# Kernel optimization log

Measured on AMD Instinct MI355X. Metric: run time of the kernel, lower is better.

Reference implementation:

```python
import jax, jax.numpy as jnp
import numpy as np

N, B, H, D = 8, 4, 16, 64   # batch, beam, heads, head_dim
T, S, L = 16, 1024, 1024    # new tokens, prefix len, past len
E = H * D
SCALE = 1.0 / np.sqrt(D).astype(np.float32)


def setup_inputs() -> dict:
    key = jax.random.key(0)
    ks = jax.random.split(key, 10)
    wscale = 1.0 / np.sqrt(E).astype(np.float32)
    return {
        "hidden_states": jax.random.normal(ks[0], (N * B, T, E), jnp.float32),
        "attention_mask": jnp.zeros((N * B, 1, 1, S + L + T), jnp.float32),
        "rel_pos": jax.random.normal(ks[1], (N * B, H, T, S + L + T), jnp.float32) * 0.1,
        "past_prefix_key": jax.random.normal(ks[2], (N, H, S, D), jnp.float32),
        "past_prefix_value": jax.random.normal(ks[3], (N, H, S, D), jnp.float32),
        "past_key": jax.random.normal(ks[4], (N * B, H, L, D), jnp.float32),
        "past_value": jax.random.normal(ks[5], (N * B, H, L, D), jnp.float32),
        "Wq": jax.random.normal(ks[6], (E, E), jnp.float32) * wscale,
        "bq": jnp.zeros((E,), jnp.float32),
        "Wk": jax.random.normal(ks[7], (E, E), jnp.float32) * wscale,
        "bk": jnp.zeros((E,), jnp.float32),
        "Wv": jax.random.normal(ks[8], (E, E), jnp.float32) * wscale,
        "bv": jnp.zeros((E,), jnp.float32),
    }


def _heads(x):
    # (NB, T, E) -> (NB, H, T, D)
    nb, t, _ = x.shape
    return x.reshape(nb, t, H, D).transpose(0, 2, 1, 3)


def reference(hidden_states, attention_mask, rel_pos, past_prefix_key,
              past_prefix_value, past_key, past_value, Wq, bq, Wk, bk, Wv, bv):
    q = _heads(hidden_states @ Wq.T + bq)   # (NB,H,T,D)
    k = _heads(hidden_states @ Wk.T + bk)
    v = _heads(hidden_states @ Wv.T + bv)

    # prefix scores: batch-shared prefix KV, per-beam queries
    q5 = q.reshape(N, B, H, T, D)
    prefix_scores = jnp.einsum('bxhtd,bhsd->bxhts', q5, past_prefix_key)
    prefix_scores = prefix_scores.reshape(N * B, H, T, S) * SCALE

    key_layer = jnp.concatenate([past_key, k], axis=2)      # (NB,H,L+T,D)
    value_layer = jnp.concatenate([past_value, v], axis=2)
    scores = jnp.einsum('bhtd,bhsd->bhts', q, key_layer) * SCALE

    scores = jnp.concatenate([prefix_scores, scores], axis=-1)  # (NB,H,T,S+L+T)
    scores = scores + rel_pos + attention_mask
    probs = jax.nn.softmax(scores, axis=-1)

    prefix_probs = probs[..., :S]
    rest_probs = probs[..., S:]

    prefix_ctx = jnp.einsum('bxhts,bhsd->bxhtd',
                            prefix_probs.reshape(N, B, H, T, S),
                            past_prefix_value).reshape(N * B, H, T, D)
    ctx = prefix_ctx + jnp.einsum('bhts,bhsd->bhtd', rest_probs, value_layer)

    # (NB,H,T,D) -> (NB,T,E)
    return ctx.transpose(0, 2, 1, 3).reshape(N * B, T, E)
```

## Files before the change

kernel.cpp:

```cpp
#include <hip/hip_runtime.h>

#define NH 16
#define NT 16
#define DD 64
#define SS 1024
#define LL 1024
#define TOTK 2064
#define EE 1024
#define NWAVE 8

typedef __attribute__((ext_vector_type(8))) short bf16x8;
typedef __attribute__((ext_vector_type(4))) float f32x4;

__device__ __forceinline__ unsigned short f2bf(float x) {
  union { float f; unsigned u; } v; v.f = x;
  unsigned r = v.u + 0x7fffu + ((v.u >> 16) & 1u);
  return (unsigned short)(r >> 16);
}
__device__ __forceinline__ unsigned pkbf(float a, float b) {
  unsigned r;
  asm("v_cvt_pk_bf16_f32 %0, %1, %2" : "=v"(r) : "v"(a), "v"(b));
  return r;
}
union BF8 { unsigned u[4]; bf16x8 v; };

__device__ __forceinline__ void dma16(const void* g, void* l) {
  __builtin_amdgcn_global_load_lds(
      (const __attribute__((address_space(1))) unsigned int*)g,
      (__attribute__((address_space(3))) unsigned int*)l, 16, 0, 0);
}

__global__ __launch_bounds__(256)
void proj_kernel(const float* __restrict__ hidden,
                 const float* __restrict__ Wq, const float* __restrict__ bq,
                 const float* __restrict__ Wk, const float* __restrict__ bk,
                 const float* __restrict__ Wv, const float* __restrict__ bv,
                 unsigned short* __restrict__ qws,
                 float* __restrict__ kws, float* __restrict__ vws)
{
  __shared__ alignas(16) unsigned short As[64][72];
  __shared__ alignas(16) unsigned short Bs[64][72];
  const int mtile = blockIdx.x;
  const int ntile = blockIdx.y;
  const int mat = ntile >> 4;
  const int h = ntile & 15;
  const float* Wm = (mat == 0) ? Wq : (mat == 1 ? Wk : Wv);
  const float* bm = (mat == 0) ? bq : (mat == 1 ? bk : bv);
  const int tid = threadIdx.x;
  const int lane = tid & 63, w = tid >> 6;
  const int lr = lane & 15, lg = lane >> 4;
  const int m0 = mtile * 64;

  const f32x4 fz = {0.f, 0.f, 0.f, 0.f};
  f32x4 acc[4];
  #pragma unroll
  for (int j = 0; j < 4; ++j) acc[j] = fz;

  const int srow = tid >> 4, sc4 = tid & 15;
  float4 Ar[4], Br[4];
  #pragma unroll
  for (int it = 0; it < 4; ++it) {
    Ar[it] = *(const float4*)(hidden + (m0 + srow + it * 16) * EE + sc4 * 4);
    Br[it] = *(const float4*)(Wm + (h * 64 + srow + it * 16) * EE + sc4 * 4);
  }

  for (int k0 = 0; k0 < EE; k0 += 64) {
    __syncthreads();
    #pragma unroll
    for (int it = 0; it < 4; ++it) {
      int row = srow + it * 16;
      float4 a = Ar[it], b = Br[it];
      *(uint2*)(&As[row][sc4 * 4]) = make_uint2(pkbf(a.x, a.y), pkbf(a.z, a.w));
      *(uint2*)(&Bs[row][sc4 * 4]) = make_uint2(pkbf(b.x, b.y), pkbf(b.z, b.w));
    }
    __syncthreads();
    int kn = k0 + 64;
    if (kn < EE) {
      #pragma unroll
      for (int it = 0; it < 4; ++it) {
        Ar[it] = *(const float4*)(hidden + (m0 + srow + it * 16) * EE + kn + sc4 * 4);
        Br[it] = *(const float4*)(Wm + (h * 64 + srow + it * 16) * EE + kn + sc4 * 4);
      }
    }
    #pragma unroll
    for (int hh = 0; hh < 2; ++hh) {
      bf16x8 a = *(const bf16x8*)(&As[w * 16 + lr][hh * 32 + lg * 8]);
      #pragma unroll
      for (int dt = 0; dt < 4; ++dt) {
        bf16x8 b = *(const bf16x8*)(&Bs[dt * 16 + lr][hh * 32 + lg * 8]);
        acc[dt] = __builtin_amdgcn_mfma_f32_16x16x32_bf16(a, b, acc[dt], 0, 0, 0);
      }
    }
  }

  #pragma unroll
  for (int dt = 0; dt < 4; ++dt)
    #pragma unroll
    for (int r = 0; r < 4; ++r) {
      int Mrow = m0 + w * 16 + lg * 4 + r;
      int nb = Mrow >> 4, t = Mrow & 15;
      int d = dt * 16 + lr;
      float val = acc[dt][r] + bm[h * 64 + d];
      int oi = ((nb * NH + h) * NT + t) * DD + d;
      if (mat == 0) qws[oi] = f2bf(val);
      else if (mat == 1) kws[oi] = val;
      else vws[oi] = val;
    }
}

__global__ __launch_bounds__(512, 2)
void prefix_attn_kernel(const float* __restrict__ mask, const float* __restrict__ rel,
                        const float* __restrict__ ppk, const float* __restrict__ ppv,
                        const unsigned short* __restrict__ qws,
                        float* __restrict__ pfn, float* __restrict__ pfd)
{
  __shared__ __align__(16) float SB[2 * 128 * 64];
  __shared__ __align__(16) unsigned short Pb[NWAVE][16][40];

  const int bidx = blockIdx.x;
  const int h = bidx & 15;
  const int sn = bidx >> 4;
  const int nn = sn & 7;
  const int s = sn >> 3;
  const int tid = threadIdx.x;
  const int lane = tid & 63, w = tid >> 6;
  const int lr = lane & 15, lg = lane >> 4;
  const int key0 = s * 512;

  bf16x8 aq[4][2];
  #pragma unroll
  for (int b = 0; b < 4; ++b) {
    const unsigned short* qb = qws + (((nn * 4 + b) * NH + h) * NT) * DD;
    aq[b][0] = *(const bf16x8*)(qb + lr * DD + lg * 8);
    aq[b][1] = *(const bf16x8*)(qb + lr * DD + lg * 8 + 32);
  }

  const f32x4 fz = {0.f, 0.f, 0.f, 0.f};
  f32x4 ctx[4][4];
  float ls[4][4];
  #pragma unroll
  for (int b = 0; b < 4; ++b)
    #pragma unroll
    for (int j = 0; j < 4; ++j) { ctx[b][j] = fz; ls[b][j] = 0.f; }

  auto kstage = [&](int c, int buf) {
    const float* ks = ppk + ((nn * NH + h) * SS + key0 + c * 128) * DD;
    float* Kb = SB + buf * 128 * 64;
    #pragma unroll
    for (int q = 0; q < 4; ++q) {
      int Lrow = w * 16 + q * 4 + (lane >> 4);
      int colb = (lane & 15) * 16;
      int scolb = colb ^ ((Lrow & 7) << 4);
      dma16((const char*)ks + Lrow * 256 + scolb, Kb + (w * 16 + q * 4) * 64);
    }
  };

  kstage(0, 0);
  kstage(1, 1);

  #pragma unroll
  for (int p = 0; p < 2; ++p) {
    const int cA = 2 * p;
    const int kbA = key0 + cA * 128 + w * 16;

    const float* vs = ppv + ((nn * NH + h) * SS + key0 + cA * 128) * DD;
    float vraw[32];
    #pragma unroll
    for (int dt = 0; dt < 4; ++dt)
      #pragma unroll
      for (int e = 0; e < 8; ++e) {
        int kslot = lg * 8 + e;
        int j = (kslot >> 4) * 128 + w * 16 + (kslot & 15);
        vraw[dt * 8 + e] = vs[j * DD + dt * 16 + lr];
      }

    __builtin_amdgcn_sched_barrier(0);
    asm volatile("s_waitcnt vmcnt(32)" ::: "memory");
    __builtin_amdgcn_sched_barrier(0);

    float rr[4][2][4]; float mk[4][2];
    #pragma unroll
    for (int b = 0; b < 4; ++b) {
      const float* relb = rel + (((nn * 4 + b) * NH + h) * NT) * TOTK;
      const float* mb = mask + (nn * 4 + b) * TOTK;
      #pragma unroll
      for (int r = 0; r < 4; ++r) {
        rr[b][0][r] = relb[(lg * 4 + r) * TOTK + kbA + lr];
        rr[b][1][r] = relb[(lg * 4 + r) * TOTK + kbA + 128 + lr];
      }
      mk[b][0] = mb[kbA + lr];
      mk[b][1] = mb[kbA + 128 + lr];
    }

    bf16x8 kbf[2][2];
    #pragma unroll
    for (int sub = 0; sub < 2; ++sub) {
      const char* Kb = (const char*)(SB + sub * 128 * 64);
      #pragma unroll
      for (int hh = 0; hh < 2; ++hh) {
        int c0 = (hh * 128 + lg * 32) ^ ((lr & 7) << 4);
        int c1 = (hh * 128 + lg * 32 + 16) ^ ((lr & 7) << 4);
        float4 v0 = *(const float4*)(Kb + (w * 16 + lr) * 256 + c0);
        float4 v1 = *(const float4*)(Kb + (w * 16 + lr) * 256 + c1);
        BF8 o;
        o.u[0] = pkbf(v0.x, v0.y); o.u[1] = pkbf(v0.z, v0.w);
        o.u[2] = pkbf(v1.x, v1.y); o.u[3] = pkbf(v1.z, v1.w);
        kbf[sub][hh] = o.v;
      }
    }

    __builtin_amdgcn_sched_barrier(0);
    if (p == 0) { kstage(2, 0); kstage(3, 1); }
    __builtin_amdgcn_sched_barrier(0);

    bf16x8 vb[4];
    #pragma unroll
    for (int dt = 0; dt < 4; ++dt) {
      BF8 o;
      #pragma unroll
      for (int q = 0; q < 4; ++q)
        o.u[q] = pkbf(vraw[dt * 8 + q * 2], vraw[dt * 8 + q * 2 + 1]);
      vb[dt] = o.v;
    }

    #pragma unroll
    for (int b = 0; b < 4; ++b) {
      f32x4 sA = fz, sB = fz;
      sA = __builtin_amdgcn_mfma_f32_16x16x32_bf16(aq[b][0], kbf[0][0], sA, 0, 0, 0);
      sA = __builtin_amdgcn_mfma_f32_16x16x32_bf16(aq[b][1], kbf[0][1], sA, 0, 0, 0);
      sB = __builtin_amdgcn_mfma_f32_16x16x32_bf16(aq[b][0], kbf[1][0], sB, 0, 0, 0);
      sB = __builtin_amdgcn_mfma_f32_16x16x32_bf16(aq[b][1], kbf[1][1], sB, 0, 0, 0);
      #pragma unroll
      for (int r = 0; r < 4; ++r) {
        float pA = __expf(sA[r] * 0.125f + rr[b][0][r] + mk[b][0]);
        float pB = __expf(sB[r] * 0.125f + rr[b][1][r] + mk[b][1]);
        ls[b][r] += pA + pB;
        Pb[w][lg * 4 + r][lr] = f2bf(pA);
        Pb[w][lg * 4 + r][16 + lr] = f2bf(pB);
      }
      bf16x8 pa = *(const bf16x8*)(&Pb[w][lr][lg * 8]);
      #pragma unroll
      for (int dt = 0; dt < 4; ++dt)
        ctx[b][dt] = __builtin_amdgcn_mfma_f32_16x16x32_bf16(pa, vb[dt], ctx[b][dt], 0, 0, 0);
    }
  }

  #pragma unroll
  for (int b = 0; b < 4; ++b)
    #pragma unroll
    for (int r = 0; r < 4; ++r) {
      #pragma unroll
      for (int o = 8; o >= 1; o >>= 1) ls[b][r] += __shfl_xor(ls[b][r], o, 16);
    }

  float* mgc = SB;
  float* mgl = SB + NWAVE * 16 * 64;
  for (int b = 0; b < 4; ++b) {
    __syncthreads();
    #pragma unroll
    for (int dt = 0; dt < 4; ++dt)
      #pragma unroll
      for (int r = 0; r < 4; ++r)
        mgc[(w * 16 + lg * 4 + r) * 64 + dt * 16 + lr] = ctx[b][dt][r];
    if (lr == 0) {
      #pragma unroll
      for (int r = 0; r < 4; ++r) mgl[w * 16 + lg * 4 + r] = ls[b][r];
    }
    __syncthreads();
    #pragma unroll
    for (int i = 0; i < 2; ++i) {
      int idx = i * 512 + tid;
      int t = idx >> 6, d = idx & 63;
      float num = 0.f, den = 0.f;
      #pragma unroll
      for (int ww = 0; ww < NWAVE; ++ww) {
        den += mgl[ww * 16 + t];
        num += mgc[(ww * 16 + t) * 64 + d];
      }
      pfn[((sn * 16 + h) * 4 + b) * 1024 + t * 64 + d] = num;
      if (d == 0) pfd[((sn * 16 + h) * 4 + b) * 16 + t] = den;
    }
  }
}

__global__ __launch_bounds__(512, 2)
void past_attn_kernel(const float* __restrict__ mask, const float* __restrict__ rel,
                      const float* __restrict__ pk, const float* __restrict__ pv,
                      const unsigned short* __restrict__ qws,
                      const float* __restrict__ kws, const float* __restrict__ vws,
                      const float* __restrict__ pfn, const float* __restrict__ pfd,
                      float* __restrict__ out)
{
  __shared__ __align__(16) float SB[2 * 128 * 64];
  __shared__ __align__(16) unsigned short Pb[NWAVE][16][40];

  const int wg = blockIdx.x;
  const int nb = wg >> 4, h = wg & 15;
  const int tid = threadIdx.x;
  const int lane = tid & 63, w = tid >> 6;
  const int lr = lane & 15, lg = lane >> 4;

  const unsigned short* qbase = qws + ((nb * NH + h) * NT) * DD;
  bf16x8 aq0 = *(const bf16x8*)(qbase + lr * DD + lg * 8);
  bf16x8 aq1 = *(const bf16x8*)(qbase + lr * DD + lg * 8 + 32);

  const float* relbase = rel + ((nb * NH + h) * NT) * TOTK;
  const float* mbase = mask + nb * TOTK;

  const f32x4 fz = {0.f, 0.f, 0.f, 0.f};
  f32x4 ctx[4];
  float ls[4];
  #pragma unroll
  for (int dt = 0; dt < 4; ++dt) ctx[dt] = fz;
  #pragma unroll
  for (int r = 0; r < 4; ++r) ls[r] = 0.f;

  auto kstage = [&](int c, int buf) {
    const float* ks = (c < 8) ? pk + ((nb * NH + h) * LL + c * 128) * DD
                              : kws + ((nb * NH + h) * NT) * DD;
    float* Kb = SB + buf * 128 * 64;
    #pragma unroll
    for (int q = 0; q < 4; ++q) {
      int Lrow = w * 16 + q * 4 + (lane >> 4);
      int colb = (lane & 15) * 16;
      int scolb = colb ^ ((Lrow & 7) << 4);
      int srow = (c == 8) ? (Lrow & 15) : Lrow;
      dma16((const char*)ks + srow * 256 + scolb, Kb + (w * 16 + q * 4) * 64);
    }
  };

  auto qk_sub = [&](const float* Kb, const float rr[4], float mv, int sub) {
    bf16x8 kbf[2];
    #pragma unroll
    for (int hh = 0; hh < 2; ++hh) {
      int c0 = (hh * 128 + lg * 32) ^ ((lr & 7) << 4);
      int c1 = (hh * 128 + lg * 32 + 16) ^ ((lr & 7) << 4);
      float4 v0 = *(const float4*)((const char*)Kb + (w * 16 + lr) * 256 + c0);
      float4 v1 = *(const float4*)((const char*)Kb + (w * 16 + lr) * 256 + c1);
      BF8 o;
      o.u[0] = pkbf(v0.x, v0.y); o.u[1] = pkbf(v0.z, v0.w);
      o.u[2] = pkbf(v1.x, v1.y); o.u[3] = pkbf(v1.z, v1.w);
      kbf[hh] = o.v;
    }
    f32x4 s = fz;
    s = __builtin_amdgcn_mfma_f32_16x16x32_bf16(aq0, kbf[0], s, 0, 0, 0);
    s = __builtin_amdgcn_mfma_f32_16x16x32_bf16(aq1, kbf[1], s, 0, 0, 0);
    #pragma unroll
    for (int r = 0; r < 4; ++r) {
      float p = __expf(s[r] * 0.125f + rr[r] + mv);
      ls[r] += p;
      Pb[w][lg * 4 + r][sub * 16 + lr] = f2bf(p);
    }
  };

  auto rel_load = [&](int cA, float (&rA)[4], float (&rB)[4], float& mA, float& mB) {
    int kbA = SS + cA * 128 + w * 16, kbB = kbA + 128;
    #pragma unroll
    for (int r = 0; r < 4; ++r) {
      rA[r] = relbase[(lg * 4 + r) * TOTK + kbA + lr];
      rB[r] = relbase[(lg * 4 + r) * TOTK + kbB + lr];
    }
    mA = mbase[kbA + lr];
    mB = mbase[kbB + lr];
  };

  auto pair_iter = [&](int p, float (&rA)[4], float (&rB)[4], float& mA, float& mB,
                       float (&rAn)[4], float (&rBn)[4], float& mAn, float& mBn) {
    const int cA = 2 * p;

    __builtin_amdgcn_sched_barrier(0);
    asm volatile("s_waitcnt vmcnt(10)" ::: "memory");
    __builtin_amdgcn_sched_barrier(0);

    const float* vs = pv + ((nb * NH + h) * LL + cA * 128) * DD;
    float vraw[32];
    #pragma unroll
    for (int dt = 0; dt < 4; ++dt)
      #pragma unroll
      for (int e = 0; e < 8; ++e) {
        int kslot = lg * 8 + e;
        int j = (kslot >> 4) * 128 + w * 16 + (kslot & 15);
        vraw[dt * 8 + e] = vs[j * DD + dt * 16 + lr];
      }
    __builtin_amdgcn_sched_barrier(0);

    qk_sub(SB, rA, mA, 0);
    qk_sub(SB + 128 * 64, rB, mB, 1);

    __builtin_amdgcn_sched_barrier(0);
    if (p < 3) {
      kstage(cA + 2, 0);
      kstage(cA + 3, 1);
      rel_load(cA + 2, rAn, rBn, mAn, mBn);
    } else {
      kstage(8, 0);
    }
    __builtin_amdgcn_sched_barrier(0);

    bf16x8 pa = *(const bf16x8*)(&Pb[w][lr][lg * 8]);
    #pragma unroll
    for (int dt = 0; dt < 4; ++dt) {
      BF8 o;
      #pragma unroll
      for (int q = 0; q < 4; ++q)
        o.u[q] = pkbf(vraw[dt * 8 + q * 2], vraw[dt * 8 + q * 2 + 1]);
      ctx[dt] = __builtin_amdgcn_mfma_f32_16x16x32_bf16(pa, o.v, ctx[dt], 0, 0, 0);
    }
  };

  kstage(0, 0);
  kstage(1, 1);
  float ra0[4], rb0[4], ma0, mb0, ra1[4], rb1[4], ma1, mb1;
  rel_load(0, ra0, rb0, ma0, mb0);
  ma1 = mb1 = 0.f; ra1[0]=ra1[1]=ra1[2]=ra1[3]=0.f; rb1[0]=rb1[1]=rb1[2]=rb1[3]=0.f;

  for (int p = 0; p < 4; p += 2) {
    pair_iter(p,     ra0, rb0, ma0, mb0, ra1, rb1, ma1, mb1);
    pair_iter(p + 1, ra1, rb1, ma1, mb1, ra0, rb0, ma0, mb0);
  }

  if (w == 0) {
    #pragma unroll
    for (int r = 0; r < 4; ++r) Pb[0][lg * 4 + r][16 + lr] = 0;
    const float* vs = vws + ((nb * NH + h) * NT) * DD;
    float vraw[32];
    #pragma unroll
    for (int dt = 0; dt < 4; ++dt)
      #pragma unroll
      for (int e = 0; e < 8; ++e) {
        int kslot = lg * 8 + e;
        vraw[dt * 8 + e] = (kslot < 16) ? vs[kslot * DD + dt * 16 + lr] : 0.f;
      }
    float rrT[4];
    #pragma unroll
    for (int r = 0; r < 4; ++r)
      rrT[r] = relbase[(lg * 4 + r) * TOTK + 2048 + lr];
    float mvT = mbase[2048 + lr];

    __builtin_amdgcn_sched_barrier(0);
    asm volatile("s_waitcnt vmcnt(0)" ::: "memory");
    __builtin_amdgcn_sched_barrier(0);

    qk_sub(SB, rrT, mvT, 0);

    bf16x8 pa = *(const bf16x8*)(&Pb[0][lr][lg * 8]);
    #pragma unroll
    for (int dt = 0; dt < 4; ++dt) {
      BF8 o;
      #pragma unroll
      for (int q = 0; q < 4; ++q)
        o.u[q] = pkbf(vraw[dt * 8 + q * 2], vraw[dt * 8 + q * 2 + 1]);
      ctx[dt] = __builtin_amdgcn_mfma_f32_16x16x32_bf16(pa, o.v, ctx[dt], 0, 0, 0);
    }
  }

  #pragma unroll
  for (int r = 0; r < 4; ++r) {
    #pragma unroll
    for (int o = 8; o >= 1; o >>= 1) ls[r] += __shfl_xor(ls[r], o, 16);
  }

  __syncthreads();
  float* mgc = SB;
  float* mgl = SB + NWAVE * 16 * 64;
  #pragma unroll
  for (int dt = 0; dt < 4; ++dt)
    #pragma unroll
    for (int r = 0; r < 4; ++r)
      mgc[(w * 16 + lg * 4 + r) * 64 + dt * 16 + lr] = ctx[dt][r];
  if (lr == 0) {
    #pragma unroll
    for (int r = 0; r < 4; ++r) mgl[w * 16 + lg * 4 + r] = ls[r];
  }
  __syncthreads();
  const int n = nb >> 2, b = nb & 3;
  #pragma unroll
  for (int i = 0; i < 2; ++i) {
    int idx = i * 512 + tid;
    int t = idx >> 6, d = idx & 63;
    float num = 0.f, den = 0.f;
    #pragma unroll
    for (int ww = 0; ww < NWAVE; ++ww) {
      den += mgl[ww * 16 + t];
      num += mgc[(ww * 16 + t) * 64 + d];
    }
    #pragma unroll
    for (int sp = 0; sp < 2; ++sp) {
      int pbase = (((sp * 8 + n) * 16 + h) * 4 + b);
      num += pfn[pbase * 1024 + t * 64 + d];
      den += pfd[pbase * 16 + t];
    }
    out[((nb * NT + t) * NH + h) * DD + d] = num / den;
  }
}

extern "C" void kernel_launch(void* const* d_in, const int* in_sizes, int n_in,
                              void* d_out, int out_size, void* d_ws, size_t ws_size,
                              hipStream_t stream) {
  const float* hidden = (const float*)d_in[0];
  const float* mask   = (const float*)d_in[1];
  const float* rel    = (const float*)d_in[2];
  const float* ppk    = (const float*)d_in[3];
  const float* ppv    = (const float*)d_in[4];
  const float* pk     = (const float*)d_in[5];
  const float* pv     = (const float*)d_in[6];
  const float* Wq     = (const float*)d_in[7];
  const float* bq     = (const float*)d_in[8];
  const float* Wk     = (const float*)d_in[9];
  const float* bk     = (const float*)d_in[10];
  const float* Wv     = (const float*)d_in[11];
  const float* bv     = (const float*)d_in[12];
  float* out = (float*)d_out;

  unsigned short* qws = (unsigned short*)d_ws;
  float* kws = (float*)((char*)d_ws + (1u << 20));
  float* vws = (float*)((char*)d_ws + 3u * (1u << 20));
  float* pfn = (float*)((char*)d_ws + 5u * (1u << 20));
  float* pfd = (float*)((char*)d_ws + 9u * (1u << 20));

  proj_kernel<<<dim3(8, 48), 256, 0, stream>>>(hidden, Wq, bq, Wk, bk, Wv, bv,
                                               qws, kws, vws);
  prefix_attn_kernel<<<dim3(256), 512, 0, stream>>>(mask, rel, ppk, ppv,
                                                    qws, pfn, pfd);
  past_attn_kernel<<<dim3(512), 512, 0, stream>>>(mask, rel, pk, pv,
                                                  qws, kws, vws, pfn, pfd, out);
}
```

Measured before the change: 110.0 us.

## Deepen past-attention K staging to four LDS buffers and prefetch V ahead

The past-attention kernel now keeps four K chunks in LDS and issues the K DMA for two chunks ahead. It also prefetches the next pair's V values and rel/mask into registers while the current pair is processed, aiming to hide global-load latency behind the MFMA work. This doubles LDS use to 128KB and lowers the launch bound to one block per CU, which cuts occupancy. The prefix kernel also loses its unroll and manual waitcnt scheduling in favour of a full drain per iteration, which could expose more load latency.

Result: slower. 122.6 us (+11.5%).

```diff
diff --git a/kernel.cpp b/kernel.cpp
--- a/kernel.cpp
+++ b/kernel.cpp
@@ -8,6 +8,7 @@
 #define TOTK 2064
 #define EE 1024
 #define NWAVE 8
+#define CH (128 * 64)
 
 typedef __attribute__((ext_vector_type(8))) short bf16x8;
 typedef __attribute__((ext_vector_type(4))) float f32x4;
@@ -29,6 +30,11 @@
       (const __attribute__((address_space(1))) unsigned int*)g,
       (__attribute__((address_space(3))) unsigned int*)l, 16, 0, 0);
 }
+#define SBAR() __builtin_amdgcn_sched_barrier(0)
+#define DRAIN() do { \
+    asm volatile("s_waitcnt vmcnt(0)" ::: "memory"); \
+    __builtin_amdgcn_sched_barrier(0); \
+  } while (0)
 
 __global__ __launch_bounds__(256)
 void proj_kernel(const float* __restrict__ hidden,
@@ -108,13 +114,13 @@
     }
 }
 
-__global__ __launch_bounds__(512, 2)
+__global__ __launch_bounds__(512, 1)
 void prefix_attn_kernel(const float* __restrict__ mask, const float* __restrict__ rel,
                         const float* __restrict__ ppk, const float* __restrict__ ppv,
                         const unsigned short* __restrict__ qws,
                         float* __restrict__ pfn, float* __restrict__ pfd)
 {
-  __shared__ __align__(16) float SB[2 * 128 * 64];
+  __shared__ __align__(16) float SB[2 * CH];
   __shared__ __align__(16) unsigned short Pb[NWAVE][16][40];
 
   const int bidx = blockIdx.x;
@@ -126,6 +132,7 @@
   const int lane = tid & 63, w = tid >> 6;
   const int lr = lane & 15, lg = lane >> 4;
   const int key0 = s * 512;
+  const f32x4 fz = {0.f, 0.f, 0.f, 0.f};
 
   bf16x8 aq[4][2];
   #pragma unroll
@@ -135,7 +142,6 @@
     aq[b][1] = *(const bf16x8*)(qb + lr * DD + lg * 8 + 32);
   }
 
-  const f32x4 fz = {0.f, 0.f, 0.f, 0.f};
   f32x4 ctx[4][4];
   float ls[4][4];
   #pragma unroll
@@ -145,7 +151,7 @@
 
   auto kstage = [&](int c, int buf) {
     const float* ks = ppk + ((nn * NH + h) * SS + key0 + c * 128) * DD;
-    float* Kb = SB + buf * 128 * 64;
+    float* Kb = SB + buf * CH;
     #pragma unroll
     for (int q = 0; q < 4; ++q) {
       int Lrow = w * 16 + q * 4 + (lane >> 4);
@@ -158,10 +164,11 @@
   kstage(0, 0);
   kstage(1, 1);
 
-  #pragma unroll
   for (int p = 0; p < 2; ++p) {
     const int cA = 2 * p;
     const int kbA = key0 + cA * 128 + w * 16;
+
+    DRAIN();
 
     const float* vs = ppv + ((nn * NH + h) * SS + key0 + cA * 128) * DD;
     float vraw[32];
@@ -173,11 +180,6 @@
         int j = (kslot >> 4) * 128 + w * 16 + (kslot & 15);
         vraw[dt * 8 + e] = vs[j * DD + dt * 16 + lr];
       }
-
-    __builtin_amdgcn_sched_barrier(0);
-    asm volatile("s_waitcnt vmcnt(32)" ::: "memory");
-    __builtin_amdgcn_sched_barrier(0);
-
     float rr[4][2][4]; float mk[4][2];
     #pragma unroll
     for (int b = 0; b < 4; ++b) {
@@ -195,7 +197,7 @@
     bf16x8 kbf[2][2];
     #pragma unroll
     for (int sub = 0; sub < 2; ++sub) {
-      const char* Kb = (const char*)(SB + sub * 128 * 64);
+      const char* Kb = (const char*)(SB + sub * CH);
       #pragma unroll
       for (int hh = 0; hh < 2; ++hh) {
         int c0 = (hh * 128 + lg * 32) ^ ((lr & 7) << 4);
@@ -209,9 +211,7 @@
       }
     }
 
-    __builtin_amdgcn_sched_barrier(0);
     if (p == 0) { kstage(2, 0); kstage(3, 1); }
-    __builtin_amdgcn_sched_barrier(0);
 
     bf16x8 vb[4];
     #pragma unroll
@@ -283,7 +283,7 @@
   }
 }
 
-__global__ __launch_bounds__(512, 2)
+__global__ __launch_bounds__(512, 1)
 void past_attn_kernel(const float* __restrict__ mask, const float* __restrict__ rel,
                       const float* __restrict__ pk, const float* __restrict__ pv,
                       const unsigned short* __restrict__ qws,
@@ -291,7 +291,7 @@
                       const float* __restrict__ pfn, const float* __restrict__ pfd,
                       float* __restrict__ out)
 {
-  __shared__ __align__(16) float SB[2 * 128 * 64];
+  __shared__ __align__(16) float SB[4 * CH];
   __shared__ __align__(16) unsigned short Pb[NWAVE][16][40];
 
   const int wg = blockIdx.x;
@@ -299,6 +299,7 @@
   const int tid = threadIdx.x;
   const int lane = tid & 63, w = tid >> 6;
   const int lr = lane & 15, lg = lane >> 4;
+  const f32x4 fz = {0.f, 0.f, 0.f, 0.f};
 
   const unsigned short* qbase = qws + ((nb * NH + h) * NT) * DD;
   bf16x8 aq0 = *(const bf16x8*)(qbase + lr * DD + lg * 8);
@@ -307,7 +308,6 @@
   const float* relbase = rel + ((nb * NH + h) * NT) * TOTK;
   const float* mbase = mask + nb * TOTK;
 
-  const f32x4 fz = {0.f, 0.f, 0.f, 0.f};
   f32x4 ctx[4];
   float ls[4];
   #pragma unroll
@@ -315,10 +315,10 @@
   #pragma unroll
   for (int r = 0; r < 4; ++r) ls[r] = 0.f;
 
-  auto kstage = [&](int c, int buf) {
+  auto kstage = [&](int c) {
     const float* ks = (c < 8) ? pk + ((nb * NH + h) * LL + c * 128) * DD
                               : kws + ((nb * NH + h) * NT) * DD;
-    float* Kb = SB + buf * 128 * 64;
+    float* Kb = SB + (c & 3) * CH;
     #pragma unroll
     for (int q = 0; q < 4; ++q) {
       int Lrow = w * 16 + q * 4 + (lane >> 4);
@@ -327,6 +327,18 @@
       int srow = (c == 8) ? (Lrow & 15) : Lrow;
       dma16((const char*)ks + srow * 256 + scolb, Kb + (w * 16 + q * 4) * 64);
     }
+  };
+
+  auto vload = [&](int p, float (&vraw)[32]) {
+    const float* vs = pv + ((nb * NH + h) * LL + 2 * p * 128) * DD;
+    #pragma unroll
+    for (int dt = 0; dt < 4; ++dt)
+      #pragma unroll
+      for (int e = 0; e < 8; ++e) {
+        int kslot = lg * 8 + e;
+        int j = (kslot >> 4) * 128 + w * 16 + (kslot & 15);
+        vraw[dt * 8 + e] = vs[j * DD + dt * 16 + lr];
+      }
   };
 
   auto qk_sub = [&](const float* Kb, const float rr[4], float mv, int sub) {
@@ -364,72 +376,64 @@
     mB = mbase[kbB + lr];
   };
 
-  auto pair_iter = [&](int p, float (&rA)[4], float (&rB)[4], float& mA, float& mB,
-                       float (&rAn)[4], float (&rBn)[4], float& mAn, float& mBn) {
+  auto pair_iter = [&](int p, float (&vrawC)[32], float (&rA)[4], float (&rB)[4],
+                       float& mA, float& mB,
+                       float (&vrawN)[32], float (&rAn)[4], float (&rBn)[4],
+                       float& mAn, float& mBn) {
     const int cA = 2 * p;
 
-    __builtin_amdgcn_sched_barrier(0);
-    asm volatile("s_waitcnt vmcnt(10)" ::: "memory");
-    __builtin_amdgcn_sched_barrier(0);
-
-    const float* vs = pv + ((nb * NH + h) * LL + cA * 128) * DD;
-    float vraw[32];
+    qk_sub(SB + (cA & 3) * CH, rA, mA, 0);
+    qk_sub(SB + ((cA + 1) & 3) * CH, rB, mB, 1);
+    SBAR();
+
+    if (p < 2)      { kstage(cA + 4); kstage(cA + 5); }
+    else if (p == 2){ kstage(8); }
+    SBAR();
+    if (p < 3) {
+      rel_load(cA + 2, rAn, rBn, mAn, mBn);
+      vload(p + 1, vrawN);
+    }
+    SBAR();
+
+    bf16x8 pa = *(const bf16x8*)(&Pb[w][lr][lg * 8]);
+    #pragma unroll
+    for (int dt = 0; dt < 4; ++dt) {
+      BF8 o;
+      #pragma unroll
+      for (int q = 0; q < 4; ++q)
+        o.u[q] = pkbf(vrawC[dt * 8 + q * 2], vrawC[dt * 8 + q * 2 + 1]);
+      ctx[dt] = __builtin_amdgcn_mfma_f32_16x16x32_bf16(pa, o.v, ctx[dt], 0, 0, 0);
+    }
+  };
+
+  kstage(0); kstage(1); kstage(2); kstage(3);
+  SBAR();
+  float ra0[4], rb0[4], ma0, mb0, ra1[4], rb1[4], ma1, mb1;
+  float vraw0[32], vraw1[32];
+  rel_load(0, ra0, rb0, ma0, mb0);
+  vload(0, vraw0);
+  ma1 = mb1 = 0.f; ra1[0]=ra1[1]=ra1[2]=ra1[3]=0.f; rb1[0]=rb1[1]=rb1[2]=rb1[3]=0.f;
+  #pragma unroll
+  for (int i = 0; i < 32; ++i) vraw1[i] = 0.f;
+  DRAIN();
+
+  for (int p = 0; p < 4; p += 2) {
+    pair_iter(p,     vraw0, ra0, rb0, ma0, mb0, vraw1, ra1, rb1, ma1, mb1);
+    pair_iter(p + 1, vraw1, ra1, rb1, ma1, mb1, vraw0, ra0, rb0, ma0, mb0);
+  }
+
+  if (w == 0) {
+    DRAIN();
+    #pragma unroll
+    for (int r = 0; r < 4; ++r) Pb[0][lg * 4 + r][16 + lr] = 0;
+    const float* vs = vws + ((nb * NH + h) * NT) * DD;
+    float vrawT[32];
     #pragma unroll
     for (int dt = 0; dt < 4; ++dt)
       #pragma unroll
       for (int e = 0; e < 8; ++e) {
         int kslot = lg * 8 + e;
-        int j = (kslot >> 4) * 128 + w * 16 + (kslot & 15);
-        vraw[dt * 8 + e] = vs[j * DD + dt * 16 + lr];
-      }
-    __builtin_amdgcn_sched_barrier(0);
-
-    qk_sub(SB, rA, mA, 0);
-    qk_sub(SB + 128 * 64, rB, mB, 1);
-
-    __builtin_amdgcn_sched_barrier(0);
-    if (p < 3) {
-      kstage(cA + 2, 0);
-      kstage(cA + 3, 1);
-      rel_load(cA + 2, rAn, rBn, mAn, mBn);
-    } else {
-      kstage(8, 0);
-    }
-    __builtin_amdgcn_sched_barrier(0);
-
-    bf16x8 pa = *(const bf16x8*)(&Pb[w][lr][lg * 8]);
-    #pragma unroll
-    for (int dt = 0; dt < 4; ++dt) {
-      BF8 o;
-      #pragma unroll
-      for (int q = 0; q < 4; ++q)
-        o.u[q] = pkbf(vraw[dt * 8 + q * 2], vraw[dt * 8 + q * 2 + 1]);
-      ctx[dt] = __builtin_amdgcn_mfma_f32_16x16x32_bf16(pa, o.v, ctx[dt], 0, 0, 0);
-    }
-  };
-
-  kstage(0, 0);
-  kstage(1, 1);
-  float ra0[4], rb0[4], ma0, mb0, ra1[4], rb1[4], ma1, mb1;
-  rel_load(0, ra0, rb0, ma0, mb0);
-  ma1 = mb1 = 0.f; ra1[0]=ra1[1]=ra1[2]=ra1[3]=0.f; rb1[0]=rb1[1]=rb1[2]=rb1[3]=0.f;
-
-  for (int p = 0; p < 4; p += 2) {
-    pair_iter(p,     ra0, rb0, ma0, mb0, ra1, rb1, ma1, mb1);
-    pair_iter(p + 1, ra1, rb1, ma1, mb1, ra0, rb0, ma0, mb0);
-  }
-
-  if (w == 0) {
-    #pragma unroll
-    for (int r = 0; r < 4; ++r) Pb[0][lg * 4 + r][16 + lr] = 0;
-    const float* vs = vws + ((nb * NH + h) * NT) * DD;
-    float vraw[32];
-    #pragma unroll
-    for (int dt = 0; dt < 4; ++dt)
-      #pragma unroll
-      for (int e = 0; e < 8; ++e) {
-        int kslot = lg * 8 + e;
-        vraw[dt * 8 + e] = (kslot < 16) ? vs[kslot * DD + dt * 16 + lr] : 0.f;
+        vrawT[dt * 8 + e] = (kslot < 16) ? vs[kslot * DD + dt * 16 + lr] : 0.f;
       }
     float rrT[4];
     #pragma unroll
@@ -437,10 +441,6 @@
       rrT[r] = relbase[(lg * 4 + r) * TOTK + 2048 + lr];
     float mvT = mbase[2048 + lr];
 
-    __builtin_amdgcn_sched_barrier(0);
-    asm volatile("s_waitcnt vmcnt(0)" ::: "memory");
-    __builtin_amdgcn_sched_barrier(0);
-
     qk_sub(SB, rrT, mvT, 0);
 
     bf16x8 pa = *(const bf16x8*)(&Pb[0][lr][lg * 8]);
@@ -449,7 +449,7 @@
       BF8 o;
       #pragma unroll
       for (int q = 0; q < 4; ++q)
-        o.u[q] = pkbf(vraw[dt * 8 + q * 2], vraw[dt * 8 + q * 2 + 1]);
+        o.u[q] = pkbf(vrawT[dt * 8 + q * 2], vrawT[dt * 8 + q * 2 + 1]);
       ctx[dt] = __builtin_amdgcn_mfma_f32_16x16x32_bf16(pa, o.v, ctx[dt], 0, 0, 0);
     }
   }
@@ -513,7 +513,7 @@
   float* out = (float*)d_out;
 
   unsigned short* qws = (unsigned short*)d_ws;
-  float* kws = (float*)((char*)d_ws + (1u << 20));
+  float* kws = (float*)((char*)d_ws + 1u * (1u << 20));
   float* vws = (float*)((char*)d_ws + 3u * (1u << 20));
   float* pfn = (float*)((char*)d_ws + 5u * (1u << 20));
   float* pfd = (float*)((char*)d_ws + 9u * (1u << 20));
```
